# Kernel optimization log

Measured on AMD Instinct MI355X. Metric: run time of the kernel, lower is better.

Reference implementation:

```python
import jax, jax.numpy as jnp
import numpy as np

D = 256       # video_dim == gcn_dims == interaction_dim
FD = 512      # forward_dim = 2 * interaction_dim
UPDATE_RATE = 0.5


def setup_inputs() -> dict:
    key = jax.random.key(0)
    ks = jax.random.split(key, 20)
    T, N = 768, 384
    s = lambda *sh: 1.0 / np.sqrt(sh[-1])
    return {
        "video_features": jax.random.normal(ks[0], (T, D), jnp.float32),
        "text_features": jax.random.normal(ks[1], (N, D), jnp.float32),
        "video_position_embedding": jax.random.normal(ks[2], (T, D), jnp.float32),
        "text_position_embedding": jax.random.normal(ks[3], (N, D), jnp.float32),
        # VideoEncoder conv1d (out=D, in=D, k=3)
        "conv_w": jax.random.normal(ks[4], (D, D, 3), jnp.float32) * (1.0 / np.sqrt(D * 3)),
        "conv_b": jax.random.normal(ks[5], (D,), jnp.float32) * 0.01,
        # TextGnnEncoder
        "bil_w": jax.random.normal(ks[6], (D, D), jnp.float32) * s(D, D),
        "lin_w": jax.random.normal(ks[7], (D, D), jnp.float32) * s(D, D),
        "lin_b": jax.random.normal(ks[8], (D,), jnp.float32) * 0.01,
        # PairInteraction
        "W1": jax.random.normal(ks[9], (FD, D), jnp.float32) * s(FD, D),
        "b1": jax.random.normal(ks[10], (FD,), jnp.float32) * 0.01,
        "W2": jax.random.normal(ks[11], (FD, D), jnp.float32) * s(FD, D),
        "Wi": jax.random.normal(ks[12], (D, FD), jnp.float32) * s(D, FD),
        "bi": jax.random.normal(ks[13], (D,), jnp.float32) * 0.01,
        # amplifier generators (Linear(interaction_dim, 1))
        "wt": jax.random.normal(ks[14], (D,), jnp.float32) * s(D,),
        "bt": jax.random.normal(ks[15], (1,), jnp.float32) * 0.01,
        "wv": jax.random.normal(ks[16], (D,), jnp.float32) * s(D,),
        "bv": jax.random.normal(ks[17], (1,), jnp.float32) * 0.01,
    }


def _forward(video_features, text_features, video_position_embedding, text_position_embedding,
             conv_w, conv_b, bil_w, lin_w, lin_b, W1, b1, W2, Wi, bi, wt, bt, wv, bv):
    T, N = video_features.shape[0], text_features.shape[0]
    input_video, input_text = video_features, text_features

    v = video_features + video_position_embedding          # (T, D)
    t = text_features + text_position_embedding            # (N, D)

    # VideoEncoder: Conv1d(k=3, pad=1) over time, then ReLU (dropout=0 in eval)
    x = v.T[None]                                           # (1, D, T)
    x = jax.lax.conv_general_dilated(x, conv_w, (1,), [(1, 1)],
                                     dimension_numbers=("NCH", "OIH", "NCH"))
    v = jax.nn.relu(x[0] + conv_b[:, None]).T               # (T, D)

    # TextGnnEncoder
    tn = t / jnp.maximum(jnp.linalg.norm(t, axis=1, keepdims=True), 1e-12)  # L2 normalize rows
    edges = (tn @ bil_w.T) @ tn.T                            # (N, N)
    weights = jax.nn.sigmoid(jnp.mean(edges, axis=1, keepdims=True))        # (N, 1)
    t = weights * (tn @ lin_w.T + lin_b)                     # (N, D)

    # PairInteraction: broadcast add + ReLU + Linear
    f1 = v @ W1.T + b1                                       # (T, FD)
    f2 = t @ W2.T                                            # (N, FD)
    h = jax.nn.relu(f1[:, None, :] + f2[None, :, :])         # (T, N, FD)
    imap = jnp.einsum("tnf,of->tno", h, Wi) + bi             # (T, N, D)

    # dual softmax attention pooling
    text_att = jax.nn.softmax(imap @ wt + bt, axis=1)        # (T, N), softmax over N
    text_context = jnp.einsum("tn,nd->td", text_att, t)      # (T, D)
    video_att = jax.nn.softmax(imap @ wv + bv, axis=0)       # (T, N), softmax over T
    video_context = jnp.einsum("tn,td->nd", video_att, v)    # (N, D)

    ur = UPDATE_RATE
    t_out = video_context * ur + t * (1.0 - ur) + input_text
    v_out = text_context * ur + v * (1.0 - ur) + input_video
    return v_out, t_out


def reference(video_features, text_features, video_position_embedding, text_position_embedding,
              conv_w, conv_b, bil_w, lin_w, lin_b, W1, b1, W2, Wi, bi, wt, bt, wv, bv):
    return _forward(video_features, text_features, video_position_embedding, text_position_embedding,
                    conv_w, conv_b, bil_w, lin_w, lin_b, W1, b1, W2, Wi, bi, wt, bt, wv, bv)
```

## Files before the change

### kernel.cpp

```cpp
#include <hip/hip_runtime.h>
#include <math.h>

#define D  256
#define T  768
#define N  384
#define FD 512

#define DOT4(A,B) ((A).x*(B).x + (A).y*(B).y + (A).z*(B).z + (A).w*(B).w)

__global__ __launch_bounds__(256) void k_front(
    const float* __restrict__ vf, const float* __restrict__ vpos,
    const float* __restrict__ cw,
    const float* __restrict__ tf, const float* __restrict__ tpos,
    const float* __restrict__ lin_w, const float* __restrict__ lin_b,
    const float* __restrict__ Wi, const float* __restrict__ wt,
    const float* __restrict__ wv,
    float* __restrict__ vep, float* __restrict__ tn,
    float* __restrict__ tl, float* __restrict__ ut, float* __restrict__ uv)
{
    __shared__ float smem[10880];
    const int b = blockIdx.x, tid = threadIdx.x;

    if (b < 288) {
        const int k  = b % 3;
        const int rem = b / 3;
        const int t0 = (rem % 12) * 64;
        const int o0 = (rem / 12) * 32;
        float (*As)[68] = (float(*)[68])smem;
        float (*Bs)[68] = (float(*)[68])(smem + 4352);
        const int p = tid >> 4, oi = tid & 15;
        float a00=0.f,a01=0.f,a10=0.f,a11=0.f,a20=0.f,a21=0.f,a30=0.f,a31=0.f;

        for (int c = 0; c < 4; ++c) {
            const int i0 = c << 6;
            __syncthreads();
#pragma unroll
            for (int s = 0; s < 4; ++s) {
                int u = tid + (s << 8);
                int r = u >> 4, q4 = (u & 15) * 4;
                int gr = t0 + r + k - 1;
                float4 v = make_float4(0.f,0.f,0.f,0.f);
                if (gr >= 0 && gr < T) {
                    float4 x = *(const float4*)&vf[gr*D + i0 + q4];
                    float4 y = *(const float4*)&vpos[gr*D + i0 + q4];
                    v = make_float4(x.x+y.x, x.y+y.y, x.z+y.z, x.w+y.w);
                }
                *(float4*)&As[r][q4] = v;
            }
#pragma unroll
            for (int s = 0; s < 8; ++s) {
                int u = tid + (s << 8);
                int o = u >> 6, i = u & 63;
                Bs[o][i] = cw[(o0 + o)*768 + (i0 + i)*3 + k];
            }
            __syncthreads();
#pragma unroll 4
            for (int kc4 = 0; kc4 < 16; ++kc4) {
                float4 r0 = *(const float4*)&As[4*p    ][kc4*4];
                float4 r1 = *(const float4*)&As[4*p + 1][kc4*4];
                float4 r2 = *(const float4*)&As[4*p + 2][kc4*4];
                float4 r3 = *(const float4*)&As[4*p + 3][kc4*4];
                float4 b0 = *(const float4*)&Bs[oi     ][kc4*4];
                float4 b1 = *(const float4*)&Bs[oi + 16][kc4*4];
                a00 += DOT4(r0,b0); a01 += DOT4(r0,b1);
                a10 += DOT4(r1,b0); a11 += DOT4(r1,b1);
                a20 += DOT4(r2,b0); a21 += DOT4(r2,b1);
                a30 += DOT4(r3,b0); a31 += DOT4(r3,b1);
            }
        }
        float* vz = vep + k * (T*D);
        const int t = t0 + 4*p;
        vz[(t  )*D + o0 + oi] = a00;  vz[(t  )*D + o0 + oi + 16] = a01;
        vz[(t+1)*D + o0 + oi] = a10;  vz[(t+1)*D + o0 + oi + 16] = a11;
        vz[(t+2)*D + o0 + oi] = a20;  vz[(t+2)*D + o0 + oi + 16] = a21;
        vz[(t+3)*D + o0 + oi] = a30;  vz[(t+3)*D + o0 + oi + 16] = a31;
    } else if (b < 384) {
        const int wid = tid >> 6, lane = tid & 63;
        const int r = (b - 288)*4 + wid;
        float v[4]; float ss = 0.f;
#pragma unroll
        for (int kk = 0; kk < 4; ++kk) {
            v[kk] = tf[r*D + lane + 64*kk] + tpos[r*D + lane + 64*kk];
            ss += v[kk]*v[kk];
        }
#pragma unroll
        for (int off = 1; off < 64; off <<= 1) ss += __shfl_xor(ss, off);
        float inv = 1.0f / fmaxf(sqrtf(ss), 1e-12f);
#pragma unroll
        for (int kk = 0; kk < 4; ++kk) tn[r*D + lane + 64*kk] = v[kk] * inv;
    } else if (b < 480) {
        const int bb = b - 384;
        const int n0 = (bb >> 3) * 32;
        const int o0 = (bb & 7) * 32;
        float (*As2)[260] = (float(*)[260])smem;
        float (*Bs2)[68]  = (float(*)[68])(smem + 8320);
        float* inv = smem + 10496;
#pragma unroll
        for (int s = 0; s < 8; ++s) {
            int u = tid + (s << 8);
            int r = u >> 6, q4 = (u & 63) * 4;
            float4 x = *(const float4*)&tf[(n0 + r)*D + q4];
            float4 y = *(const float4*)&tpos[(n0 + r)*D + q4];
            *(float4*)&As2[r][q4] = make_float4(x.x+y.x, x.y+y.y, x.z+y.z, x.w+y.w);
        }
        __syncthreads();
        {
            const int r = tid >> 3, j = tid & 7;
            float p = 0.f;
#pragma unroll
            for (int m = 0; m < 8; ++m) {
                float4 a = *(const float4*)&As2[r][j*32 + m*4];
                p += DOT4(a, a);
            }
            p += __shfl_xor(p, 1); p += __shfl_xor(p, 2); p += __shfl_xor(p, 4);
            if (j == 0) inv[r] = 1.0f / fmaxf(sqrtf(p), 1e-12f);
        }
        const int tA = tid >> 4, oA = tid & 15;
        float acc00=0.f, acc01=0.f, acc10=0.f, acc11=0.f;
        for (int c = 0; c < 4; ++c) {
            const int d0 = c << 6;
            __syncthreads();
#pragma unroll
            for (int s = 0; s < 2; ++s) {
                int u = tid + (s << 8);
                int o = u >> 4, q4 = (u & 15) * 4;
                *(float4*)&Bs2[o][q4] = *(const float4*)&lin_w[(o0 + o)*D + d0 + q4];
            }
            __syncthreads();
#pragma unroll 4
            for (int kc4 = 0; kc4 < 16; ++kc4) {
                float4 a0 = *(const float4*)&As2[tA     ][d0 + kc4*4];
                float4 a1 = *(const float4*)&As2[tA + 16][d0 + kc4*4];
                float4 b0 = *(const float4*)&Bs2[oA     ][kc4*4];
                float4 b1 = *(const float4*)&Bs2[oA + 16][kc4*4];
                acc00 += DOT4(a0,b0); acc01 += DOT4(a0,b1);
                acc10 += DOT4(a1,b0); acc11 += DOT4(a1,b1);
            }
        }
        const float i0n = inv[tA], i1n = inv[tA + 16];
        const float lb0 = lin_b[o0 + oA], lb1 = lin_b[o0 + oA + 16];
        tl[(n0 + tA     )*D + o0 + oA]      = i0n*acc00 + lb0;
        tl[(n0 + tA     )*D + o0 + oA + 16] = i0n*acc01 + lb1;
        tl[(n0 + tA + 16)*D + o0 + oA]      = i1n*acc10 + lb0;
        tl[(n0 + tA + 16)*D + o0 + oA + 16] = i1n*acc11 + lb1;
    } else {
        float* wsm = smem;
        const int which = b - 480;
        const float* w = (which < 2) ? wt : wv;
        float* u = (which < 2) ? ut : uv;
        const int f = ((which & 1) << 8) + tid;
        wsm[tid] = w[tid];
        __syncthreads();
        float s = 0.f;
#pragma unroll 4
        for (int d = 0; d < D; ++d) s += wsm[d] * Wi[d*FD + f];
        u[f] = s;
    }
}

__global__ __launch_bounds__(256) void k_mid(
    const float* __restrict__ vep, const float* __restrict__ cbp,
    const float* __restrict__ W1, const float* __restrict__ b1v,
    const float* __restrict__ tlp, const float* __restrict__ W2,
    const float* __restrict__ tn, const float* __restrict__ bil,
    float* __restrict__ f1, float* __restrict__ f2,
    float* __restrict__ ve, float* __restrict__ q)
{
    __shared__ float smem[6656];
    const int b = blockIdx.x, tid = threadIdx.x;

    if (b < 288) {
        const bool isF1 = (b < 192);
        const int bb = isF1 ? b : b - 192;
        const int nT = isF1 ? 12 : 6;
        const int r0 = (bb % nT) * 64;
        const int f0 = (bb / nT) * 32;
        float (*As)[68] = (float(*)[68])smem;
        float (*Bs)[68] = (float(*)[68])(smem + 4352);
        const int p = tid >> 4, fi = tid & 15;
        float a00=0.f,a01=0.f,a10=0.f,a11=0.f,a20=0.f,a21=0.f,a30=0.f,a31=0.f;
        const float* Wp = isF1 ? W1 : W2;

        for (int c = 0; c < 4; ++c) {
            const int d0 = c << 6;
            __syncthreads();
            if (isF1) {
#pragma unroll
                for (int s = 0; s < 4; ++s) {
                    int u = tid + (s << 8);
                    int r = u >> 4, q4 = (u & 15) * 4;
                    const int off = (r0 + r)*D + d0 + q4;
                    float4 p0 = *(const float4*)&vep[off];
                    float4 p1 = *(const float4*)&vep[T*D + off];
                    float4 p2 = *(const float4*)&vep[2*T*D + off];
                    float4 cbv = *(const float4*)&cbp[d0 + q4];
                    float4 v;
                    v.x = fmaxf(p0.x+p1.x+p2.x+cbv.x, 0.f);
                    v.y = fmaxf(p0.y+p1.y+p2.y+cbv.y, 0.f);
                    v.z = fmaxf(p0.z+p1.z+p2.z+cbv.z, 0.f);
                    v.w = fmaxf(p0.w+p1.w+p2.w+cbv.w, 0.f);
                    *(float4*)&As[r][q4] = v;
                }
            } else {
#pragma unroll
                for (int s = 0; s < 4; ++s) {
                    int u = tid + (s << 8);
                    int r = u >> 4, q4 = (u & 15) * 4;
                    *(float4*)&As[r][q4] = *(const float4*)&tlp[(r0 + r)*D + d0 + q4];
                }
            }
#pragma unroll
            for (int s = 0; s < 2; ++s) {
                int u = tid + (s << 8);
                int o = u >> 4, q4 = (u & 15) * 4;
                *(float4*)&Bs[o][q4] = *(const float4*)&Wp[(f0 + o)*D + d0 + q4];
            }
            __syncthreads();
#pragma unroll 4
            for (int kc4 = 0; kc4 < 16; ++kc4) {
                float4 r0v = *(const float4*)&As[4*p    ][kc4*4];
                float4 r1v = *(const float4*)&As[4*p + 1][kc4*4];
                float4 r2v = *(const float4*)&As[4*p + 2][kc4*4];
                float4 r3v = *(const float4*)&As[4*p + 3][kc4*4];
                float4 b0 = *(const float4*)&Bs[fi     ][kc4*4];
                float4 b1 = *(const float4*)&Bs[fi + 16][kc4*4];
                a00 += DOT4(r0v,b0); a01 += DOT4(r0v,b1);
                a10 += DOT4(r1v,b0); a11 += DOT4(r1v,b1);
                a20 += DOT4(r2v,b0); a21 += DOT4(r2v,b1);
                a30 += DOT4(r3v,b0); a31 += DOT4(r3v,b1);
            }
        }
        const int r = r0 + 4*p;
        if (isF1) {
            const float bi0 = b1v[f0 + fi], bi1 = b1v[f0 + fi + 16];
            f1[(r  )*FD + f0 + fi] = a00 + bi0;  f1[(r  )*FD + f0 + fi + 16] = a01 + bi1;
            f1[(r+1)*FD + f0 + fi] = a10 + bi0;  f1[(r+1)*FD + f0 + fi + 16] = a11 + bi1;
            f1[(r+2)*FD + f0 + fi] = a20 + bi0;  f1[(r+2)*FD + f0 + fi + 16] = a21 + bi1;
            f1[(r+3)*FD + f0 + fi] = a30 + bi0;  f1[(r+3)*FD + f0 + fi + 16] = a31 + bi1;
        } else {
            f2[(r  )*FD + f0 + fi] = a00;  f2[(r  )*FD + f0 + fi + 16] = a01;
            f2[(r+1)*FD + f0 + fi] = a10;  f2[(r+1)*FD + f0 + fi + 16] = a11;
            f2[(r+2)*FD + f0 + fi] = a20;  f2[(r+2)*FD + f0 + fi + 16] = a21;
            f2[(r+3)*FD + f0 + fi] = a30;  f2[(r+3)*FD + f0 + fi + 16] = a31;
        }
    } else if (b < 384) {
        const int t0 = (b - 288) * 8;
        float cbv = cbp[tid];
#pragma unroll
        for (int r = 0; r < 8; ++r) {
            const int off = (t0 + r)*D + tid;
            float s = vep[off] + vep[T*D + off] + vep[2*T*D + off] + cbv;
            ve[off] = fmaxf(s, 0.f);
        }
    } else {
        float* tb = smem;
        float (*qp)[32] = (float(*)[32])(smem + 256);
        const int bq = b - 384;
        float s = 0.f;
#pragma unroll 8
        for (int n = 0; n < N; ++n) s += tn[n*D + tid];
        tb[tid] = s * (1.0f / (float)N);
        __syncthreads();
        const int o = tid & 31, dg = tid >> 5;
        float p = 0.f;
#pragma unroll 8
        for (int d = dg*32; d < dg*32 + 32; ++d) p += tb[d] * bil[d*D + bq*32 + o];
        qp[dg][o] = p;
        __syncthreads();
        if (tid < 32) {
            float acc = 0.f;
#pragma unroll
            for (int kk = 0; kk < 8; ++kk) acc += qp[kk][tid];
            q[bq*32 + tid] = acc;
        }
    }
}

__global__ __launch_bounds__(256) void k_score(
    const float* __restrict__ f1, const float* __restrict__ f2,
    const float* __restrict__ tn, const float* __restrict__ qv,
    const float* __restrict__ tlp,
    const float* __restrict__ ut, const float* __restrict__ uv,
    float* __restrict__ stp, float* __restrict__ svp, float* __restrict__ tg)
{
    __shared__ float smem[5152];
    const int tid = threadIdx.x;
    const int bid = blockIdx.x;

    if (bid < 576) {
        const int t0 = (bid % 24) * 32;
        const int n0 = ((bid / 24) % 12) * 32;
        const int iz = bid / 288;
        const int fh = iz * 256;
        float (*f1s)[68] = (float(*)[68])smem;
        float (*f2s)[68] = (float(*)[68])(smem + 2176);
        float* us_t = smem + 4352;
        float* us_v = smem + 4608;
        float* qs   = smem + 4864;
        float* wsm  = smem + 5120;

        qs[tid]   = qv[tid];
        us_t[tid] = ut[fh + tid];
        us_v[tid] = uv[fh + tid];
        __syncthreads();
        {
            const int r = tid >> 3, j = tid & 7;
            float p = 0.f;
#pragma unroll
            for (int m = 0; m < 8; ++m) {
                float4 a = *(const float4*)&tn[(n0 + r)*D + j*32 + m*4];
                float4 qq = *(const float4*)&qs[j*32 + m*4];
                p += DOT4(a, qq);
            }
            p += __shfl_xor(p, 1); p += __shfl_xor(p, 2); p += __shfl_xor(p, 4);
            if (j == 0) wsm[r] = 1.0f / (1.0f + expf(-p));
        }

        const int ti = tid >> 4, ni = tid & 15;
        float at[2][2] = {{0.f,0.f},{0.f,0.f}};
        float av[2][2] = {{0.f,0.f},{0.f,0.f}};

        for (int c = 0; c < 4; ++c) {
            const int f00 = fh + c*64;
            __syncthreads();
#pragma unroll
            for (int s = 0; s < 2; ++s) {
                int u = tid + (s << 8);
                int r = u >> 4, q4 = (u & 15) * 4;
                *(float4*)&f1s[r][q4] = *(const float4*)&f1[(t0 + r)*FD + f00 + q4];
                float w = wsm[r];
                float4 v = *(const float4*)&f2[(n0 + r)*FD + f00 + q4];
                *(float4*)&f2s[r][q4] = make_float4(w*v.x, w*v.y, w*v.z, w*v.w);
            }
            __syncthreads();
#pragma unroll 4
            for (int fq = 0; fq < 16; ++fq) {
                float utv[4], uvv[4], a0[4], a1[4], b0[4], b1[4];
                *(float4*)utv = *(const float4*)&us_t[c*64 + fq*4];
                *(float4*)uvv = *(const float4*)&us_v[c*64 + fq*4];
                *(float4*)a0  = *(const float4*)&f1s[ti     ][fq*4];
                *(float4*)a1  = *(const float4*)&f1s[ti + 16][fq*4];
                *(float4*)b0  = *(const float4*)&f2s[ni     ][fq*4];
                *(float4*)b1  = *(const float4*)&f2s[ni + 16][fq*4];
#pragma unroll
                for (int e = 0; e < 4; ++e) {
                    float h00 = fmaxf(a0[e] + b0[e], 0.f);
                    float h01 = fmaxf(a0[e] + b1[e], 0.f);
                    float h10 = fmaxf(a1[e] + b0[e], 0.f);
                    float h11 = fmaxf(a1[e] + b1[e], 0.f);
                    at[0][0] += h00*utv[e]; av[0][0] += h00*uvv[e];
                    at[0][1] += h01*utv[e]; av[0][1] += h01*uvv[e];
                    at[1][0] += h10*utv[e]; av[1][0] += h10*uvv[e];
                    at[1][1] += h11*utv[e]; av[1][1] += h11*uvv[e];
                }
            }
        }
        __syncthreads();
#pragma unroll
        for (int i = 0; i < 2; ++i)
#pragma unroll
            for (int j = 0; j < 2; ++j) {
                f1s[ti + 16*i][ni + 16*j] = at[i][j];
                f2s[ni + 16*j][ti + 16*i] = av[i][j];
            }
        __syncthreads();
        float* stz = stp + iz * (T*N);
        float* svz = svp + iz * (N*T);
        {
            const int row = tid >> 3, c4 = (tid & 7) * 4;
            *(float4*)&stz[(t0 + row)*N + n0 + c4] = *(const float4*)&f1s[row][c4];
            *(float4*)&svz[(n0 + row)*T + t0 + c4] = *(const float4*)&f2s[row][c4];
        }
    } else {
        const int n0 = (bid - 576) * 32;
        float* qs  = smem;
        float* wsm = smem + 256;
        qs[tid] = qv[tid];
        __syncthreads();
        {
            const int r = tid >> 3, j = tid & 7;
            float p = 0.f;
#pragma unroll
            for (int m = 0; m < 8; ++m) {
                float4 a = *(const float4*)&tn[(n0 + r)*D + j*32 + m*4];
                float4 qq = *(const float4*)&qs[j*32 + m*4];
                p += DOT4(a, qq);
            }
            p += __shfl_xor(p, 1); p += __shfl_xor(p, 2); p += __shfl_xor(p, 4);
            if (j == 0) wsm[r] = 1.0f / (1.0f + expf(-p));
        }
        __syncthreads();
#pragma unroll
        for (int r = 0; r < 32; ++r)
            tg[(n0 + r)*D + tid] = wsm[r] * tlp[(n0 + r)*D + tid];
    }
}

__global__ __launch_bounds__(256) void k_att(
    const float* __restrict__ stp, const float* __restrict__ svp,
    const float* __restrict__ tg, const float* __restrict__ ve,
    const float* __restrict__ vf, const float* __restrict__ tf,
    float* __restrict__ out_v, float* __restrict__ out_t)
{
    __shared__ float attb[768][8];
    __shared__ float red[4][8];
    __shared__ float ptA[4][8][64];
    __shared__ float ptB[4][8][64];
    const int tid = threadIdx.x;
    const int oo = tid & 63, g = tid >> 6;
    const int TN = T*N;

    if (blockIdx.x < 192) {
        const int bx = blockIdx.x >> 1, h = blockIdx.x & 1;
        const int t0 = bx * 8;
        const int oA = h*128 + oo, oB = oA + 64;

        float v1[8], v2[8];
#pragma unroll
        for (int r = 0; r < 8; ++r) {
            const float* p = stp + (t0 + r)*N + tid;
            v1[r] = p[0] + p[TN];
            v2[r] = (tid < 128) ? (p[256] + p[TN + 256]) : -1e30f;
        }
        float m[8], si[8];
#pragma unroll
        for (int r = 0; r < 8; ++r) {
            float mm = fmaxf(v1[r], v2[r]);
#pragma unroll
            for (int off = 1; off < 64; off <<= 1) mm = fmaxf(mm, __shfl_xor(mm, off));
            if (oo == 0) red[g][r] = mm;
        }
        __syncthreads();
#pragma unroll
        for (int r = 0; r < 8; ++r)
            m[r] = fmaxf(fmaxf(red[0][r], red[1][r]), fmaxf(red[2][r], red[3][r]));
        __syncthreads();
        float e1[8], e2[8];
#pragma unroll
        for (int r = 0; r < 8; ++r) {
            e1[r] = expf(v1[r] - m[r]);
            e2[r] = (tid < 128) ? expf(v2[r] - m[r]) : 0.f;
            float ss = e1[r] + e2[r];
#pragma unroll
            for (int off = 1; off < 64; off <<= 1) ss += __shfl_xor(ss, off);
            if (oo == 0) red[g][r] = ss;
        }
        __syncthreads();
#pragma unroll
        for (int r = 0; r < 8; ++r)
            si[r] = 1.0f / (red[0][r] + red[1][r] + red[2][r] + red[3][r]);
#pragma unroll
        for (int r = 0; r < 8; ++r) {
            attb[tid][r] = e1[r] * si[r];
            if (tid < 128) attb[tid + 256][r] = e2[r] * si[r];
        }
        __syncthreads();

        float accA[8] = {0.f,0.f,0.f,0.f,0.f,0.f,0.f,0.f};
        float accB[8] = {0.f,0.f,0.f,0.f,0.f,0.f,0.f,0.f};
#pragma unroll 4
        for (int n = g; n < N; n += 4) {
            float4 a0 = *(const float4*)&attb[n][0];
            float4 a1 = *(const float4*)&attb[n][4];
            float tvA = tg[n*D + oA], tvB = tg[n*D + oB];
            accA[0] += a0.x*tvA; accA[1] += a0.y*tvA; accA[2] += a0.z*tvA; accA[3] += a0.w*tvA;
            accA[4] += a1.x*tvA; accA[5] += a1.y*tvA; accA[6] += a1.z*tvA; accA[7] += a1.w*tvA;
            accB[0] += a0.x*tvB; accB[1] += a0.y*tvB; accB[2] += a0.z*tvB; accB[3] += a0.w*tvB;
            accB[4] += a1.x*tvB; accB[5] += a1.y*tvB; accB[6] += a1.z*tvB; accB[7] += a1.w*tvB;
        }
#pragma unroll
        for (int r = 0; r < 8; ++r) { ptA[g][r][oo] = accA[r]; ptB[g][r][oo] = accB[r]; }
        __syncthreads();
#pragma unroll
        for (int rr = g; rr < 8; rr += 4) {
            float sA = ptA[0][rr][oo] + ptA[1][rr][oo] + ptA[2][rr][oo] + ptA[3][rr][oo];
            float sB = ptB[0][rr][oo] + ptB[1][rr][oo] + ptB[2][rr][oo] + ptB[3][rr][oo];
            int t = t0 + rr;
            out_v[t*D + oA] = 0.5f*sA + 0.5f*ve[t*D + oA] + vf[t*D + oA];
            out_v[t*D + oB] = 0.5f*sB + 0.5f*ve[t*D + oB] + vf[t*D + oB];
        }
    } else {
        const int b2 = blockIdx.x - 192;
        const int bx = b2 >> 1, h = b2 & 1;
        const int n0 = bx * 8;
        const int oA = h*128 + oo, oB = oA + 64;

        float v1[8], v2[8], v3[8];
#pragma unroll
        for (int r = 0; r < 8; ++r) {
            const float* p = svp + (n0 + r)*T + tid;
            v1[r] = p[0]   + p[TN];
            v2[r] = p[256] + p[TN + 256];
            v3[r] = p[512] + p[TN + 512];
        }
        float m[8], si[8];
#pragma unroll
        for (int r = 0; r < 8; ++r) {
            float mm = fmaxf(fmaxf(v1[r], v2[r]), v3[r]);
#pragma unroll
            for (int off = 1; off < 64; off <<= 1) mm = fmaxf(mm, __shfl_xor(mm, off));
            if (oo == 0) red[g][r] = mm;
        }
        __syncthreads();
#pragma unroll
        for (int r = 0; r < 8; ++r)
            m[r] = fmaxf(fmaxf(red[0][r], red[1][r]), fmaxf(red[2][r], red[3][r]));
        __syncthreads();
        float e1[8], e2[8], e3[8];
#pragma unroll
        for (int r = 0; r < 8; ++r) {
            e1[r] = expf(v1[r] - m[r]);
            e2[r] = expf(v2[r] - m[r]);
            e3[r] = expf(v3[r] - m[r]);
            float ss = e1[r] + e2[r] + e3[r];
#pragma unroll
            for (int off = 1; off < 64; off <<= 1) ss += __shfl_xor(ss, off);
            if (oo == 0) red[g][r] = ss;
        }
        __syncthreads();
#pragma unroll
        for (int r = 0; r < 8; ++r)
            si[r] = 1.0f / (red[0][r] + red[1][r] + red[2][r] + red[3][r]);
#pragma unroll
        for (int r = 0; r < 8; ++r) {
            attb[tid][r]       = e1[r] * si[r];
            attb[tid + 256][r] = e2[r] * si[r];
            attb[tid + 512][r] = e3[r] * si[r];
        }
        __syncthreads();

        float accA[8] = {0.f,0.f,0.f,0.f,0.f,0.f,0.f,0.f};
        float accB[8] = {0.f,0.f,0.f,0.f,0.f,0.f,0.f,0.f};
#pragma unroll 4
        for (int t = g; t < T; t += 4) {
            float4 a0 = *(const float4*)&attb[t][0];
            float4 a1 = *(const float4*)&attb[t][4];
            float vvA = ve[t*D + oA], vvB = ve[t*D + oB];
            accA[0] += a0.x*vvA; accA[1] += a0.y*vvA; accA[2] += a0.z*vvA; accA[3] += a0.w*vvA;
            accA[4] += a1.x*vvA; accA[5] += a1.y*vvA; accA[6] += a1.z*vvA; accA[7] += a1.w*vvA;
            accB[0] += a0.x*vvB; accB[1] += a0.y*vvB; accB[2] += a0.z*vvB; accB[3] += a0.w*vvB;
            accB[4] += a1.x*vvB; accB[5] += a1.y*vvB; accB[6] += a1.z*vvB; accB[7] += a1.w*vvB;
        }
#pragma unroll
        for (int r = 0; r < 8; ++r) { ptA[g][r][oo] = accA[r]; ptB[g][r][oo] = accB[r]; }
        __syncthreads();
#pragma unroll
        for (int rr = g; rr < 8; rr += 4) {
            float sA = ptA[0][rr][oo] + ptA[1][rr][oo] + ptA[2][rr][oo] + ptA[3][rr][oo];
            float sB = ptB[0][rr][oo] + ptB[1][rr][oo] + ptB[2][rr][oo] + ptB[3][rr][oo];
            int n = n0 + rr;
            out_t[n*D + oA] = 0.5f*sA + 0.5f*tg[n*D + oA] + tf[n*D + oA];
            out_t[n*D + oB] = 0.5f*sB + 0.5f*tg[n*D + oB] + tf[n*D + oB];
        }
    }
}

extern "C" void kernel_launch(void* const* d_in, const int* in_sizes, int n_in,
                              void* d_out, int out_size, void* d_ws, size_t ws_size,
                              hipStream_t stream)
{
    (void)in_sizes; (void)n_in; (void)out_size; (void)ws_size;
    const float* vf   = (const float*)d_in[0];
    const float* tf   = (const float*)d_in[1];
    const float* vpos = (const float*)d_in[2];
    const float* tpos = (const float*)d_in[3];
    const float* cw   = (const float*)d_in[4];
    const float* cb   = (const float*)d_in[5];
    const float* bil  = (const float*)d_in[6];
    const float* lw   = (const float*)d_in[7];
    const float* lb   = (const float*)d_in[8];
    const float* W1   = (const float*)d_in[9];
    const float* b1   = (const float*)d_in[10];
    const float* W2   = (const float*)d_in[11];
    const float* Wi   = (const float*)d_in[12];
    const float* wt   = (const float*)d_in[14];
    const float* wv   = (const float*)d_in[16];

    float* ws  = (float*)d_ws;
    float* vep = ws;
    float* ve  = vep + 3*T*D;
    float* tn  = ve + T*D;
    float* tl  = tn + N*D;
    float* tg  = tl + N*D;
    float* f1  = tg + N*D;
    float* f2  = f1 + T*FD;
    float* q   = f2 + N*FD;
    float* ut  = q + D;
    float* uv  = ut + FD;
    float* stp = uv + FD;
    float* svp = stp + 2*T*N;

    float* out_v = (float*)d_out;
    float* out_t = out_v + T*D;

    hipLaunchKernelGGL(k_front, dim3(484), dim3(256), 0, stream,
                       vf, vpos, cw, tf, tpos, lw, lb, Wi, wt, wv, vep, tn, tl, ut, uv);
    hipLaunchKernelGGL(k_mid,   dim3(392), dim3(256), 0, stream,
                       vep, cb, W1, b1, tl, W2, tn, bil, f1, f2, ve, q);
    hipLaunchKernelGGL(k_score, dim3(588), dim3(256), 0, stream,
                       f1, f2, tn, q, tl, ut, uv, stp, svp, tg);
    hipLaunchKernelGGL(k_att,   dim3(288), dim3(256), 0, stream,
                       stp, svp, tg, ve, vf, tf, out_v, out_t);
}
```

Baseline: 99.88 us.

## Stream GEMM operands from global memory instead of LDS staging across kernels

Adds a pre-pass kernel that writes a zero-padded sum of video features and position embeddings, so the conv blocks read shifted rows straight from global memory. The conv, linear, W1/W2 projection and score stages stop staging one operand through LDS in 64-wide chunks. They now load the whole weight or f2 tile into LDS once, or read it directly from global or cache, which removes per-chunk barriers. The costs are an extra kernel launch, an extra padded buffer, and uncoalesced, redundant global reads per thread that rely on the cache.

```diff
diff --git a/kernel.cpp b/kernel.cpp
--- a/kernel.cpp
+++ b/kernel.cpp
@@ -8,9 +8,25 @@
 
 #define DOT4(A,B) ((A).x*(B).x + (A).y*(B).y + (A).z*(B).z + (A).w*(B).w)
 
+__global__ __launch_bounds__(256) void k_vpe(
+    const float* __restrict__ vf, const float* __restrict__ vpos,
+    float* __restrict__ vpe)
+{
+    const int tid = threadIdx.x;
+    const int r0 = blockIdx.x * 8;
+#pragma unroll
+    for (int s = 0; s < 8; ++s) {
+        int r = r0 + s;
+        if (r < 770) {
+            float v = 0.f;
+            if (r >= 1 && r <= T) v = vf[(r-1)*D + tid] + vpos[(r-1)*D + tid];
+            vpe[r*D + tid] = v;
+        }
+    }
+}
+
 __global__ __launch_bounds__(256) void k_front(
-    const float* __restrict__ vf, const float* __restrict__ vpos,
-    const float* __restrict__ cw,
+    const float* __restrict__ vpe, const float* __restrict__ cw,
     const float* __restrict__ tf, const float* __restrict__ tpos,
     const float* __restrict__ lin_w, const float* __restrict__ lin_b,
     const float* __restrict__ Wi, const float* __restrict__ wt,
@@ -26,47 +42,30 @@
         const int rem = b / 3;
         const int t0 = (rem % 12) * 64;
         const int o0 = (rem / 12) * 32;
-        float (*As)[68] = (float(*)[68])smem;
-        float (*Bs)[68] = (float(*)[68])(smem + 4352);
+        float (*Bs)[260] = (float(*)[260])smem;
+#pragma unroll
+        for (int s = 0; s < 32; ++s) {
+            int u = tid + (s << 8);
+            int o = u >> 8, i = u & 255;
+            Bs[o][i] = cw[(o0 + o)*768 + i*3 + k];
+        }
+        __syncthreads();
+
         const int p = tid >> 4, oi = tid & 15;
+        const float* ar = vpe + (t0 + 4*p + k)*D;
         float a00=0.f,a01=0.f,a10=0.f,a11=0.f,a20=0.f,a21=0.f,a30=0.f,a31=0.f;
-
-        for (int c = 0; c < 4; ++c) {
-            const int i0 = c << 6;
-            __syncthreads();
-#pragma unroll
-            for (int s = 0; s < 4; ++s) {
-                int u = tid + (s << 8);
-                int r = u >> 4, q4 = (u & 15) * 4;
-                int gr = t0 + r + k - 1;
-                float4 v = make_float4(0.f,0.f,0.f,0.f);
-                if (gr >= 0 && gr < T) {
-                    float4 x = *(const float4*)&vf[gr*D + i0 + q4];
-                    float4 y = *(const float4*)&vpos[gr*D + i0 + q4];
-                    v = make_float4(x.x+y.x, x.y+y.y, x.z+y.z, x.w+y.w);
-                }
-                *(float4*)&As[r][q4] = v;
-            }
-#pragma unroll
-            for (int s = 0; s < 8; ++s) {
-                int u = tid + (s << 8);
-                int o = u >> 6, i = u & 63;
-                Bs[o][i] = cw[(o0 + o)*768 + (i0 + i)*3 + k];
-            }
-            __syncthreads();
-#pragma unroll 4
-            for (int kc4 = 0; kc4 < 16; ++kc4) {
-                float4 r0 = *(const float4*)&As[4*p    ][kc4*4];
-                float4 r1 = *(const float4*)&As[4*p + 1][kc4*4];
-                float4 r2 = *(const float4*)&As[4*p + 2][kc4*4];
-                float4 r3 = *(const float4*)&As[4*p + 3][kc4*4];
-                float4 b0 = *(const float4*)&Bs[oi     ][kc4*4];
-                float4 b1 = *(const float4*)&Bs[oi + 16][kc4*4];
-                a00 += DOT4(r0,b0); a01 += DOT4(r0,b1);
-                a10 += DOT4(r1,b0); a11 += DOT4(r1,b1);
-                a20 += DOT4(r2,b0); a21 += DOT4(r2,b1);
-                a30 += DOT4(r3,b0); a31 += DOT4(r3,b1);
-            }
+#pragma unroll 4
+        for (int fq = 0; fq < 64; ++fq) {
+            float4 r0 = *(const float4*)&ar[          fq*4];
+            float4 r1 = *(const float4*)&ar[    D   + fq*4];
+            float4 r2 = *(const float4*)&ar[ 2*D    + fq*4];
+            float4 r3 = *(const float4*)&ar[ 3*D    + fq*4];
+            float4 b0 = *(const float4*)&Bs[oi     ][fq*4];
+            float4 b1 = *(const float4*)&Bs[oi + 16][fq*4];
+            a00 += DOT4(r0,b0); a01 += DOT4(r0,b1);
+            a10 += DOT4(r1,b0); a11 += DOT4(r1,b1);
+            a20 += DOT4(r2,b0); a21 += DOT4(r2,b1);
+            a30 += DOT4(r3,b0); a31 += DOT4(r3,b1);
         }
         float* vz = vep + k * (T*D);
         const int t = t0 + 4*p;
@@ -93,8 +92,7 @@
         const int n0 = (bb >> 3) * 32;
         const int o0 = (bb & 7) * 32;
         float (*As2)[260] = (float(*)[260])smem;
-        float (*Bs2)[68]  = (float(*)[68])(smem + 8320);
-        float* inv = smem + 10496;
+        float* inv = smem + 8320;
 #pragma unroll
         for (int s = 0; s < 8; ++s) {
             int u = tid + (s << 8);
@@ -115,27 +113,19 @@
             p += __shfl_xor(p, 1); p += __shfl_xor(p, 2); p += __shfl_xor(p, 4);
             if (j == 0) inv[r] = 1.0f / fmaxf(sqrtf(p), 1e-12f);
         }
+        __syncthreads();
         const int tA = tid >> 4, oA = tid & 15;
+        const float* lr0 = lin_w + (o0 + oA)*D;
+        const float* lr1 = lin_w + (o0 + oA + 16)*D;
         float acc00=0.f, acc01=0.f, acc10=0.f, acc11=0.f;
-        for (int c = 0; c < 4; ++c) {
-            const int d0 = c << 6;
-            __syncthreads();
-#pragma unroll
-            for (int s = 0; s < 2; ++s) {
-                int u = tid + (s << 8);
-                int o = u >> 4, q4 = (u & 15) * 4;
-                *(float4*)&Bs2[o][q4] = *(const float4*)&lin_w[(o0 + o)*D + d0 + q4];
-            }
-            __syncthreads();
-#pragma unroll 4
-            for (int kc4 = 0; kc4 < 16; ++kc4) {
-                float4 a0 = *(const float4*)&As2[tA     ][d0 + kc4*4];
-                float4 a1 = *(const float4*)&As2[tA + 16][d0 + kc4*4];
-                float4 b0 = *(const float4*)&Bs2[oA     ][kc4*4];
-                float4 b1 = *(const float4*)&Bs2[oA + 16][kc4*4];
-                acc00 += DOT4(a0,b0); acc01 += DOT4(a0,b1);
-                acc10 += DOT4(a1,b0); acc11 += DOT4(a1,b1);
-            }
+#pragma unroll 4
+        for (int kc4 = 0; kc4 < 64; ++kc4) {
+            float4 a0 = *(const float4*)&As2[tA     ][kc4*4];
+            float4 a1 = *(const float4*)&As2[tA + 16][kc4*4];
+            float4 b0 = *(const float4*)&lr0[kc4*4];
+            float4 b1 = *(const float4*)&lr1[kc4*4];
+            acc00 += DOT4(a0,b0); acc01 += DOT4(a0,b1);
+            acc10 += DOT4(a1,b0); acc11 += DOT4(a1,b1);
         }
         const float i0n = inv[tA], i1n = inv[tA + 16];
         const float lb0 = lin_b[o0 + oA], lb1 = lin_b[o0 + oA + 16];
@@ -166,7 +156,7 @@
     float* __restrict__ f1, float* __restrict__ f2,
     float* __restrict__ ve, float* __restrict__ q)
 {
-    __shared__ float smem[6656];
+    __shared__ float smem[4352];
     const int b = blockIdx.x, tid = threadIdx.x;
 
     if (b < 288) {
@@ -176,10 +166,11 @@
         const int r0 = (bb % nT) * 64;
         const int f0 = (bb / nT) * 32;
         float (*As)[68] = (float(*)[68])smem;
-        float (*Bs)[68] = (float(*)[68])(smem + 4352);
         const int p = tid >> 4, fi = tid & 15;
+        const float* Wp = isF1 ? W1 : W2;
+        const float* Wr0 = Wp + (f0 + fi)*D;
+        const float* Wr1 = Wp + (f0 + fi + 16)*D;
         float a00=0.f,a01=0.f,a10=0.f,a11=0.f,a20=0.f,a21=0.f,a30=0.f,a31=0.f;
-        const float* Wp = isF1 ? W1 : W2;
 
         for (int c = 0; c < 4; ++c) {
             const int d0 = c << 6;
@@ -209,21 +200,15 @@
                     *(float4*)&As[r][q4] = *(const float4*)&tlp[(r0 + r)*D + d0 + q4];
                 }
             }
-#pragma unroll
-            for (int s = 0; s < 2; ++s) {
-                int u = tid + (s << 8);
-                int o = u >> 4, q4 = (u & 15) * 4;
-                *(float4*)&Bs[o][q4] = *(const float4*)&Wp[(f0 + o)*D + d0 + q4];
-            }
             __syncthreads();
 #pragma unroll 4
             for (int kc4 = 0; kc4 < 16; ++kc4) {
+                float4 b0 = *(const float4*)&Wr0[d0 + kc4*4];
+                float4 b1 = *(const float4*)&Wr1[d0 + kc4*4];
                 float4 r0v = *(const float4*)&As[4*p    ][kc4*4];
                 float4 r1v = *(const float4*)&As[4*p + 1][kc4*4];
                 float4 r2v = *(const float4*)&As[4*p + 2][kc4*4];
                 float4 r3v = *(const float4*)&As[4*p + 3][kc4*4];
-                float4 b0 = *(const float4*)&Bs[fi     ][kc4*4];
-                float4 b1 = *(const float4*)&Bs[fi + 16][kc4*4];
                 a00 += DOT4(r0v,b0); a01 += DOT4(r0v,b1);
                 a10 += DOT4(r1v,b0); a11 += DOT4(r1v,b1);
                 a20 += DOT4(r2v,b0); a21 += DOT4(r2v,b1);
@@ -283,7 +268,7 @@
     const float* __restrict__ ut, const float* __restrict__ uv,
     float* __restrict__ stp, float* __restrict__ svp, float* __restrict__ tg)
 {
-    __shared__ float smem[5152];
+    __shared__ float smem[8608];
     const int tid = threadIdx.x;
     const int bid = blockIdx.x;
 
@@ -292,16 +277,11 @@
         const int n0 = ((bid / 24) % 12) * 32;
         const int iz = bid / 288;
         const int fh = iz * 256;
-        float (*f1s)[68] = (float(*)[68])smem;
-        float (*f2s)[68] = (float(*)[68])(smem + 2176);
-        float* us_t = smem + 4352;
-        float* us_v = smem + 4608;
-        float* qs   = smem + 4864;
-        float* wsm  = smem + 5120;
-
-        qs[tid]   = qv[tid];
-        us_t[tid] = ut[fh + tid];
-        us_v[tid] = uv[fh + tid];
+        float* qs  = smem;
+        float* wsm = smem + 256;
+        float (*f2s)[260] = (float(*)[260])(smem + 288);
+
+        qs[tid] = qv[tid];
         __syncthreads();
         {
             const int r = tid >> 3, j = tid & 7;
@@ -315,61 +295,65 @@
             p += __shfl_xor(p, 1); p += __shfl_xor(p, 2); p += __shfl_xor(p, 4);
             if (j == 0) wsm[r] = 1.0f / (1.0f + expf(-p));
         }
+        __syncthreads();
+#pragma unroll
+        for (int s = 0; s < 8; ++s) {
+            int u = tid + (s << 8);
+            int r = u >> 6, q4 = (u & 63) * 4;
+            float w = wsm[r];
+            float4 v = *(const float4*)&f2[(n0 + r)*FD + fh + q4];
+            *(float4*)&f2s[r][q4] = make_float4(w*v.x, w*v.y, w*v.z, w*v.w);
+        }
+        __syncthreads();
 
         const int ti = tid >> 4, ni = tid & 15;
-        float at[2][2] = {{0.f,0.f},{0.f,0.f}};
-        float av[2][2] = {{0.f,0.f},{0.f,0.f}};
-
-        for (int c = 0; c < 4; ++c) {
-            const int f00 = fh + c*64;
-            __syncthreads();
-#pragma unroll
-            for (int s = 0; s < 2; ++s) {
-                int u = tid + (s << 8);
-                int r = u >> 4, q4 = (u & 15) * 4;
-                *(float4*)&f1s[r][q4] = *(const float4*)&f1[(t0 + r)*FD + f00 + q4];
-                float w = wsm[r];
-                float4 v = *(const float4*)&f2[(n0 + r)*FD + f00 + q4];
-                *(float4*)&f2s[r][q4] = make_float4(w*v.x, w*v.y, w*v.z, w*v.w);
+        const float* f1r0 = f1 + (t0 + ti     )*FD + fh;
+        const float* f1r1 = f1 + (t0 + ti + 16)*FD + fh;
+        const float* utp = ut + fh;
+        const float* uvp = uv + fh;
+        float at00=0.f, at01=0.f, at10=0.f, at11=0.f;
+        float av00=0.f, av01=0.f, av10=0.f, av11=0.f;
+
+#pragma unroll 4
+        for (int fq = 0; fq < 64; ++fq) {
+            float4 a0 = *(const float4*)&f1r0[fq*4];
+            float4 a1 = *(const float4*)&f1r1[fq*4];
+            float4 b0 = *(const float4*)&f2s[ni     ][fq*4];
+            float4 b1 = *(const float4*)&f2s[ni + 16][fq*4];
+            float4 uT = *(const float4*)&utp[fq*4];
+            float4 uV = *(const float4*)&uvp[fq*4];
+            const float* a0e = (const float*)&a0;
+            const float* a1e = (const float*)&a1;
+            const float* b0e = (const float*)&b0;
+            const float* b1e = (const float*)&b1;
+            const float* uTe = (const float*)&uT;
+            const float* uVe = (const float*)&uV;
+#pragma unroll
+            for (int e = 0; e < 4; ++e) {
+                float h00 = fmaxf(a0e[e] + b0e[e], 0.f);
+                float h01 = fmaxf(a0e[e] + b1e[e], 0.f);
+                float h10 = fmaxf(a1e[e] + b0e[e], 0.f);
+                float h11 = fmaxf(a1e[e] + b1e[e], 0.f);
+                at00 += h00*uTe[e]; av00 += h00*uVe[e];
+                at01 += h01*uTe[e]; av01 += h01*uVe[e];
+                at10 += h10*uTe[e]; av10 += h10*uVe[e];
+                at11 += h11*uTe[e]; av11 += h11*uVe[e];
             }
-            __syncthreads();
-#pragma unroll 4
-            for (int fq = 0; fq < 16; ++fq) {
-                float utv[4], uvv[4], a0[4], a1[4], b0[4], b1[4];
-                *(float4*)utv = *(const float4*)&us_t[c*64 + fq*4];
-                *(float4*)uvv = *(const float4*)&us_v[c*64 + fq*4];
-                *(float4*)a0  = *(const float4*)&f1s[ti     ][fq*4];
-                *(float4*)a1  = *(const float4*)&f1s[ti + 16][fq*4];
-                *(float4*)b0  = *(const float4*)&f2s[ni     ][fq*4];
-                *(float4*)b1  = *(const float4*)&f2s[ni + 16][fq*4];
-#pragma unroll
-                for (int e = 0; e < 4; ++e) {
-                    float h00 = fmaxf(a0[e] + b0[e], 0.f);
-                    float h01 = fmaxf(a0[e] + b1[e], 0.f);
-                    float h10 = fmaxf(a1[e] + b0[e], 0.f);
-                    float h11 = fmaxf(a1[e] + b1[e], 0.f);
-                    at[0][0] += h00*utv[e]; av[0][0] += h00*uvv[e];
-                    at[0][1] += h01*utv[e]; av[0][1] += h01*uvv[e];
-                    at[1][0] += h10*utv[e]; av[1][0] += h10*uvv[e];
-                    at[1][1] += h11*utv[e]; av[1][1] += h11*uvv[e];
-                }
-            }
-        }
-        __syncthreads();
-#pragma unroll
-        for (int i = 0; i < 2; ++i)
-#pragma unroll
-            for (int j = 0; j < 2; ++j) {
-                f1s[ti + 16*i][ni + 16*j] = at[i][j];
-                f2s[ni + 16*j][ti + 16*i] = av[i][j];
-            }
+        }
+        __syncthreads();
+        float (*trA)[68] = (float(*)[68])(smem + 288);
+        float (*trB)[68] = (float(*)[68])(smem + 288 + 2176);
+        trA[ti     ][ni     ] = at00;  trA[ti     ][ni + 16] = at01;
+        trA[ti + 16][ni     ] = at10;  trA[ti + 16][ni + 16] = at11;
+        trB[ni     ][ti     ] = av00;  trB[ni + 16][ti     ] = av01;
+        trB[ni     ][ti + 16] = av10;  trB[ni + 16][ti + 16] = av11;
         __syncthreads();
         float* stz = stp + iz * (T*N);
         float* svz = svp + iz * (N*T);
         {
             const int row = tid >> 3, c4 = (tid & 7) * 4;
-            *(float4*)&stz[(t0 + row)*N + n0 + c4] = *(const float4*)&f1s[row][c4];
-            *(float4*)&svz[(n0 + row)*T + t0 + c4] = *(const float4*)&f2s[row][c4];
+            *(float4*)&stz[(t0 + row)*N + n0 + c4] = *(const float4*)&trA[row][c4];
+            *(float4*)&svz[(n0 + row)*T + t0 + c4] = *(const float4*)&trB[row][c4];
         }
     } else {
         const int n0 = (bid - 576) * 32;
@@ -576,25 +560,27 @@
     const float* wt   = (const float*)d_in[14];
     const float* wv   = (const float*)d_in[16];
 
-    float* ws  = (float*)d_ws;
-    float* vep = ws;
-    float* ve  = vep + 3*T*D;
-    float* tn  = ve + T*D;
-    float* tl  = tn + N*D;
-    float* tg  = tl + N*D;
-    float* f1  = tg + N*D;
-    float* f2  = f1 + T*FD;
-    float* q   = f2 + N*FD;
-    float* ut  = q + D;
-    float* uv  = ut + FD;
-    float* stp = uv + FD;
-    float* svp = stp + 2*T*N;
+    float* ws   = (float*)d_ws;
+    float* vpe  = ws;
+    float* vep  = vpe + 770*D;
+    float* ve   = vep + 3*T*D;
+    float* tn   = ve + T*D;
+    float* tl   = tn + N*D;
+    float* tg   = tl + N*D;
+    float* f1   = tg + N*D;
+    float* f2   = f1 + T*FD;
+    float* q    = f2 + N*FD;
+    float* ut   = q + D;
+    float* uv   = ut + FD;
+    float* stp  = uv + FD;
+    float* svp  = stp + 2*T*N;
 
     float* out_v = (float*)d_out;
     float* out_t = out_v + T*D;
 
+    hipLaunchKernelGGL(k_vpe,   dim3(97),  dim3(256), 0, stream, vf, vpos, vpe);
     hipLaunchKernelGGL(k_front, dim3(484), dim3(256), 0, stream,
-                       vf, vpos, cw, tf, tpos, lw, lb, Wi, wt, wv, vep, tn, tl, ut, uv);
+                       vpe, cw, tf, tpos, lw, lb, Wi, wt, wv, vep, tn, tl, ut, uv);
     hipLaunchKernelGGL(k_mid,   dim3(392), dim3(256), 0, stream,
                        vep, cb, W1, b1, tl, W2, tn, bil, f1, f2, ve, q);
     hipLaunchKernelGGL(k_score, dim3(588), dim3(256), 0, stream,
```

After: 120.5 us. 20.6% more time.

## Remove split-K partial score buffers and compute full FD per block

Applied to the files above, without the earlier changes.

Each k_score tile block now reduces over all 512 forward dims instead of half, writing final scores directly rather than two partial planes. k_att reads a single score buffer and skips the partial-sum addition. This removes intermediate global traffic and extra reads, but halves the block count of the dominant score kernel, reducing occupancy and load balance on the GPU.

```diff
diff --git a/kernel.cpp b/kernel.cpp
--- a/kernel.cpp
+++ b/kernel.cpp
@@ -178,8 +178,8 @@
         float (*As)[68] = (float(*)[68])smem;
         float (*Bs)[68] = (float(*)[68])(smem + 4352);
         const int p = tid >> 4, fi = tid & 15;
+        const float* Wp = isF1 ? W1 : W2;
         float a00=0.f,a01=0.f,a10=0.f,a11=0.f,a20=0.f,a21=0.f,a30=0.f,a31=0.f;
-        const float* Wp = isF1 ? W1 : W2;
 
         for (int c = 0; c < 4; ++c) {
             const int d0 = c << 6;
@@ -281,27 +281,24 @@
     const float* __restrict__ tn, const float* __restrict__ qv,
     const float* __restrict__ tlp,
     const float* __restrict__ ut, const float* __restrict__ uv,
-    float* __restrict__ stp, float* __restrict__ svp, float* __restrict__ tg)
+    float* __restrict__ st, float* __restrict__ sv, float* __restrict__ tg)
 {
-    __shared__ float smem[5152];
+    __shared__ float smem[5664];
     const int tid = threadIdx.x;
     const int bid = blockIdx.x;
 
-    if (bid < 576) {
+    if (bid < 288) {
         const int t0 = (bid % 24) * 32;
-        const int n0 = ((bid / 24) % 12) * 32;
-        const int iz = bid / 288;
-        const int fh = iz * 256;
+        const int n0 = (bid / 24) * 32;
         float (*f1s)[68] = (float(*)[68])smem;
         float (*f2s)[68] = (float(*)[68])(smem + 2176);
         float* us_t = smem + 4352;
-        float* us_v = smem + 4608;
-        float* qs   = smem + 4864;
-        float* wsm  = smem + 5120;
-
-        qs[tid]   = qv[tid];
-        us_t[tid] = ut[fh + tid];
-        us_v[tid] = uv[fh + tid];
+        float* us_v = smem + 4864;
+        float* qs   = smem + 4352;
+        float* wsm  = smem + 5376;
+        qs = smem + 5408;
+
+        qs[tid] = qv[tid];
         __syncthreads();
         {
             const int r = tid >> 3, j = tid & 7;
@@ -315,13 +312,15 @@
             p += __shfl_xor(p, 1); p += __shfl_xor(p, 2); p += __shfl_xor(p, 4);
             if (j == 0) wsm[r] = 1.0f / (1.0f + expf(-p));
         }
+        us_t[tid] = ut[tid]; us_t[tid + 256] = ut[tid + 256];
+        us_v[tid] = uv[tid]; us_v[tid + 256] = uv[tid + 256];
 
         const int ti = tid >> 4, ni = tid & 15;
-        float at[2][2] = {{0.f,0.f},{0.f,0.f}};
-        float av[2][2] = {{0.f,0.f},{0.f,0.f}};
-
-        for (int c = 0; c < 4; ++c) {
-            const int f00 = fh + c*64;
+        float at00=0.f, at01=0.f, at10=0.f, at11=0.f;
+        float av00=0.f, av01=0.f, av10=0.f, av11=0.f;
+
+        for (int c = 0; c < 8; ++c) {
+            const int f00 = c*64;
             __syncthreads();
 #pragma unroll
             for (int s = 0; s < 2; ++s) {
@@ -336,8 +335,8 @@
 #pragma unroll 4
             for (int fq = 0; fq < 16; ++fq) {
                 float utv[4], uvv[4], a0[4], a1[4], b0[4], b1[4];
-                *(float4*)utv = *(const float4*)&us_t[c*64 + fq*4];
-                *(float4*)uvv = *(const float4*)&us_v[c*64 + fq*4];
+                *(float4*)utv = *(const float4*)&us_t[f00 + fq*4];
+                *(float4*)uvv = *(const float4*)&us_v[f00 + fq*4];
                 *(float4*)a0  = *(const float4*)&f1s[ti     ][fq*4];
                 *(float4*)a1  = *(const float4*)&f1s[ti + 16][fq*4];
                 *(float4*)b0  = *(const float4*)&f2s[ni     ][fq*4];
@@ -348,31 +347,28 @@
                     float h01 = fmaxf(a0[e] + b1[e], 0.f);
                     float h10 = fmaxf(a1[e] + b0[e], 0.f);
                     float h11 = fmaxf(a1[e] + b1[e], 0.f);
-                    at[0][0] += h00*utv[e]; av[0][0] += h00*uvv[e];
-                    at[0][1] += h01*utv[e]; av[0][1] += h01*uvv[e];
-                    at[1][0] += h10*utv[e]; av[1][0] += h10*uvv[e];
-                    at[1][1] += h11*utv[e]; av[1][1] += h11*uvv[e];
+                    at00 += h00*utv[e]; av00 += h00*uvv[e];
+                    at01 += h01*utv[e]; av01 += h01*uvv[e];
+                    at10 += h10*utv[e]; av10 += h10*uvv[e];
+                    at11 += h11*utv[e]; av11 += h11*uvv[e];
                 }
             }
         }
         __syncthreads();
-#pragma unroll
-        for (int i = 0; i < 2; ++i)
-#pragma unroll
-            for (int j = 0; j < 2; ++j) {
-                f1s[ti + 16*i][ni + 16*j] = at[i][j];
-                f2s[ni + 16*j][ti + 16*i] = av[i][j];
-            }
-        __syncthreads();
-        float* stz = stp + iz * (T*N);
-        float* svz = svp + iz * (N*T);
+        float (*trA)[68] = f1s;
+        float (*trB)[68] = f2s;
+        trA[ti     ][ni     ] = at00;  trA[ti     ][ni + 16] = at01;
+        trA[ti + 16][ni     ] = at10;  trA[ti + 16][ni + 16] = at11;
+        trB[ni     ][ti     ] = av00;  trB[ni + 16][ti     ] = av01;
+        trB[ni     ][ti + 16] = av10;  trB[ni + 16][ti + 16] = av11;
+        __syncthreads();
         {
             const int row = tid >> 3, c4 = (tid & 7) * 4;
-            *(float4*)&stz[(t0 + row)*N + n0 + c4] = *(const float4*)&f1s[row][c4];
-            *(float4*)&svz[(n0 + row)*T + t0 + c4] = *(const float4*)&f2s[row][c4];
+            *(float4*)&st[(t0 + row)*N + n0 + c4] = *(const float4*)&trA[row][c4];
+            *(float4*)&sv[(n0 + row)*T + t0 + c4] = *(const float4*)&trB[row][c4];
         }
     } else {
-        const int n0 = (bid - 576) * 32;
+        const int n0 = (bid - 288) * 32;
         float* qs  = smem;
         float* wsm = smem + 256;
         qs[tid] = qv[tid];
@@ -397,7 +393,7 @@
 }
 
 __global__ __launch_bounds__(256) void k_att(
-    const float* __restrict__ stp, const float* __restrict__ svp,
+    const float* __restrict__ st, const float* __restrict__ sv,
     const float* __restrict__ tg, const float* __restrict__ ve,
     const float* __restrict__ vf, const float* __restrict__ tf,
     float* __restrict__ out_v, float* __restrict__ out_t)
@@ -408,7 +404,6 @@
     __shared__ float ptB[4][8][64];
     const int tid = threadIdx.x;
     const int oo = tid & 63, g = tid >> 6;
-    const int TN = T*N;
 
     if (blockIdx.x < 192) {
         const int bx = blockIdx.x >> 1, h = blockIdx.x & 1;
@@ -418,9 +413,9 @@
         float v1[8], v2[8];
 #pragma unroll
         for (int r = 0; r < 8; ++r) {
-            const float* p = stp + (t0 + r)*N + tid;
-            v1[r] = p[0] + p[TN];
-            v2[r] = (tid < 128) ? (p[256] + p[TN + 256]) : -1e30f;
+            const float* p = st + (t0 + r)*N + tid;
+            v1[r] = p[0];
+            v2[r] = (tid < 128) ? p[256] : -1e30f;
         }
         float m[8], si[8];
 #pragma unroll
@@ -488,10 +483,10 @@
         float v1[8], v2[8], v3[8];
 #pragma unroll
         for (int r = 0; r < 8; ++r) {
-            const float* p = svp + (n0 + r)*T + tid;
-            v1[r] = p[0]   + p[TN];
-            v2[r] = p[256] + p[TN + 256];
-            v3[r] = p[512] + p[TN + 512];
+            const float* p = sv + (n0 + r)*T + tid;
+            v1[r] = p[0];
+            v2[r] = p[256];
+            v3[r] = p[512];
         }
         float m[8], si[8];
 #pragma unroll
@@ -587,8 +582,8 @@
     float* q   = f2 + N*FD;
     float* ut  = q + D;
     float* uv  = ut + FD;
-    float* stp = uv + FD;
-    float* svp = stp + 2*T*N;
+    float* st  = uv + FD;
+    float* sv  = st + T*N;
 
     float* out_v = (float*)d_out;
     float* out_t = out_v + T*D;
@@ -597,8 +592,8 @@
                        vf, vpos, cw, tf, tpos, lw, lb, Wi, wt, wv, vep, tn, tl, ut, uv);
     hipLaunchKernelGGL(k_mid,   dim3(392), dim3(256), 0, stream,
                        vep, cb, W1, b1, tl, W2, tn, bil, f1, f2, ve, q);
-    hipLaunchKernelGGL(k_score, dim3(588), dim3(256), 0, stream,
-                       f1, f2, tn, q, tl, ut, uv, stp, svp, tg);
+    hipLaunchKernelGGL(k_score, dim3(300), dim3(256), 0, stream,
+                       f1, f2, tn, q, tl, ut, uv, st, sv, tg);
     hipLaunchKernelGGL(k_att,   dim3(288), dim3(256), 0, stream,
-                       stp, svp, tg, ve, vf, tf, out_v, out_t);
+                       st, sv, tg, ve, vf, tf, out_v, out_t);
 }
```

New measurement: 107.0 us. +7.1%, slower.
